# Kernel optimization log

Hardware: AMD Instinct MI355X
Metric: run time of the kernel (lower is better)

The kernel has to match this reference:

```python
import jax, jax.numpy as jnp
import numpy as np

B = 64        # graphs per batch
N0 = 131072   # total nodes (2048 per graph)
E = 1048576   # total edges (within-graph)
H = 128       # hidden_size
C = 7         # class_num (input feature dim)
EPS = 1e-5


def setup_inputs() -> dict:
    key = jax.random.key(0)
    ks = jax.random.split(key, 16)
    n0 = N0 // B
    x = jax.random.normal(ks[0], (N0, C), dtype=jnp.float32)
    # within-graph random edges: edge e belongs to graph e // (E//B)
    g = jnp.repeat(jnp.arange(B, dtype=jnp.int32), E // B)
    row = jax.random.randint(ks[1], (E,), 0, n0, dtype=jnp.int32) + g * n0
    col = jax.random.randint(ks[2], (E,), 0, n0, dtype=jnp.int32) + g * n0
    edge_index = jnp.stack([row, col], axis=0)
    batch = jnp.repeat(jnp.arange(B, dtype=jnp.int32), n0)
    s = 0.05
    params = dict(
        Wc1=jax.random.normal(ks[3], (C, H), jnp.float32) * s,     # conv1 weight
        Wc=jax.random.normal(ks[4], (3, H, H), jnp.float32) * s,   # conv2-4 weights
        bc=jax.random.normal(ks[5], (4, H), jnp.float32) * s,      # conv biases
        Wf=jax.random.normal(ks[6], (4, H, H), jnp.float32) * s,   # fc weights
        bf=jax.random.normal(ks[7], (4, H), jnp.float32) * s,      # fc biases
        bn_g=jnp.ones((4, H), jnp.float32),                        # BN gamma
        bn_b=jnp.zeros((4, H), jnp.float32),                       # BN beta
        Ws1=jax.random.normal(ks[8], (4, H, 1), jnp.float32) * s,  # SAG GraphConv root weight
        Ws2=jax.random.normal(ks[9], (4, H, 1), jnp.float32) * s,  # SAG GraphConv neighbor weight
        bs=jax.random.normal(ks[10], (4, 1), jnp.float32) * s,     # SAG GraphConv bias
    )
    return dict(x=x, edge_index=edge_index, batch=batch, **params)


def _gcn_conv(x, W, b, row, col, m, N):
    # PyG GCNConv with self loops: out_i = sum_{j->i} h_j / sqrt(d_i d_j) + h_i / d_i + b
    h = x @ W
    deg = jax.ops.segment_sum(m, col, num_segments=N) + 1.0  # +1 for self loop
    dis = jax.lax.rsqrt(deg)
    norm = dis[row] * dis[col] * m  # masked-out edges contribute 0
    agg = jax.ops.segment_sum(h[row] * norm[:, None], col, num_segments=N)
    return agg + h * (dis * dis)[:, None] + b


def _sag_score(x, W1, W2, b, row, col, m, N):
    # GraphConv(H, 1, aggr='add'): score_i = W1^T x_i + W2^T sum_{j->i} x_j + b
    nbr = jax.ops.segment_sum(x[row] * m[:, None], col, num_segments=N)
    return (x @ W1 + nbr @ W2 + b).reshape(-1)


def _bn(x, g, b):
    mu = jnp.mean(x, axis=0)
    var = jnp.mean((x - mu) ** 2, axis=0)  # biased, matches torch BN training
    return (x - mu) * jax.lax.rsqrt(var + EPS) * g + b


def reference(x, edge_index, batch, Wc1, Wc, bc, Wf, bf, bn_g, bn_b, Ws1, Ws2, bs):
    row, col = edge_index[0], edge_index[1]
    m = jnp.ones(row.shape, x.dtype)  # edge validity mask (static-size edge list)
    n = x.shape[0] // B               # nodes per graph (equal-size graphs)
    for i in range(4):
        N = B * n
        W = Wc1 if i == 0 else Wc[i - 1]
        h = _gcn_conv(x, W, bc[i], row, col, m, N)
        h = jax.nn.relu(h @ Wf[i] + bf[i])
        h = _bn(h, bn_g[i], bn_b[i])
        # SAGPooling(ratio=0.5): per-graph top-k by GraphConv score, x *= tanh(score)
        score = _sag_score(h, Ws1[i], Ws2[i], bs[i], row, col, m, N)
        k = n // 2
        _, idx = jax.lax.top_k(score.reshape(B, n), k)  # [B, k] per-graph indices
        perm = (idx + jnp.arange(B, dtype=idx.dtype)[:, None] * n).reshape(-1)
        x = h[perm] * jnp.tanh(score[perm])[:, None]
        # re-index edges; mask edges touching removed nodes
        inv = jnp.full((N,), -1, dtype=row.dtype).at[perm].set(
            jnp.arange(B * k, dtype=row.dtype))
        nr, nc = inv[row], inv[col]
        valid = (nr >= 0) & (nc >= 0)
        m = m * valid.astype(m.dtype)
        row = jnp.where(valid, nr, 0)
        col = jnp.where(valid, nc, 0)
        n = k
    # global_mean_pool over block-structured batch -> [B, H]
    return x.reshape(B, n, -1).mean(axis=1)
```

## Files before the change

kernel.cpp:

```cpp
#include <hip/hip_runtime.h>
#include <cstdint>

#define HB 128
#define NB 64
#define NE 1048576
#define EG (NE / 256)
#define XP 132

typedef float v2f __attribute__((ext_vector_type(2)));

__global__ __launch_bounds__(256) void init_edges_k(const int* __restrict__ ei,
    int* __restrict__ row, int* __restrict__ col, int* __restrict__ gcnt0,
    int* __restrict__ ecnt0, int E) {
  int e = blockIdx.x * blockDim.x + threadIdx.x;
  if (e < E) { row[e] = ei[e]; col[e] = ei[E + e]; }
  if (blockIdx.x == 0) {
    if (threadIdx.x < NB) gcnt0[threadIdx.x] = E / NB;
    if (threadIdx.x == 0) *ecnt0 = E;
  }
}

__global__ __launch_bounds__(256) void conv_fc0_k(const float* __restrict__ aggx,
    const float* __restrict__ Wc1, const float* __restrict__ bc0,
    const float* __restrict__ Wf, const float* __restrict__ bf0,
    float* __restrict__ out, int N, float* __restrict__ stat) {
  __shared__ float lt[64][128];
  __shared__ float laggx[64][8];
  __shared__ float lwc1[7 * 128];
  float2 (*red)[128] = (float2(*)[128])lt;
  int tid = threadIdx.x;
  int tx = tid & 31, ty = tid >> 5;
  long rowbase = (long)blockIdx.x * 64;
  for (int i = tid; i < 7 * 32; i += 256)
    ((float4*)lwc1)[i] = ((const float4*)Wc1)[i];
  if (tid < 128) {
    int lr = tid >> 1, lq = (tid & 1) * 4;
    *(float4*)&laggx[lr][lq] = *(const float4*)(aggx + (rowbase + lr) * 8 + lq);
  }
  __syncthreads();
  float4 tacc[8];
  float4 bcv = ((const float4*)bc0)[tx];
  #pragma unroll
  for (int r = 0; r < 8; ++r) tacc[r] = bcv;
  #pragma unroll
  for (int k = 0; k < 7; ++k) {
    float4 wv = ((float4*)lwc1)[k * 32 + tx];
    #pragma unroll
    for (int r = 0; r < 8; ++r) {
      float xv = laggx[ty + 8 * r][k];
      tacc[r].x += xv * wv.x; tacc[r].y += xv * wv.y;
      tacc[r].z += xv * wv.z; tacc[r].w += xv * wv.w;
    }
  }
  #pragma unroll
  for (int r = 0; r < 8; ++r)
    *(float4*)&lt[ty + 8 * r][4 * tx] = tacc[r];
  __syncthreads();
  v2f acc2[16];
  #pragma unroll
  for (int r = 0; r < 16; ++r) acc2[r] = (v2f){0.f, 0.f};
  for (int kc = 0; kc < 16; ++kc) {
    float4 wreg[8];
    #pragma unroll
    for (int k = 0; k < 8; ++k)
      wreg[k] = *(const float4*)(Wf + (size_t)(kc * 8 + k) * HB + 4 * tx);
    #pragma unroll
    for (int kk = 0; kk < 8; kk += 4) {
      float4 xreg[8];
      #pragma unroll
      for (int r = 0; r < 8; ++r)
        xreg[r] = *(const float4*)&lt[ty + 8 * r][kc * 8 + kk];
      #pragma unroll
      for (int k2 = 0; k2 < 4; ++k2) {
        float4 wv = wreg[kk + k2];
        v2f wlo = {wv.x, wv.y}, whi = {wv.z, wv.w};
        #pragma unroll
        for (int r = 0; r < 8; ++r) {
          float xv = ((const float*)&xreg[r])[k2];
          v2f xvv = {xv, xv};
          acc2[2 * r]     += xvv * wlo;
          acc2[2 * r + 1] += xvv * whi;
        }
      }
    }
  }
  float4 bv = ((const float4*)bf0)[tx];
  float4 psum = make_float4(0.f, 0.f, 0.f, 0.f);
  float4 psq  = make_float4(0.f, 0.f, 0.f, 0.f);
  __syncthreads();
  #pragma unroll
  for (int r = 0; r < 8; ++r) {
    float4 v;
    v.x = fmaxf(acc2[2 * r].x + bv.x, 0.f);
    v.y = fmaxf(acc2[2 * r].y + bv.y, 0.f);
    v.z = fmaxf(acc2[2 * r + 1].x + bv.z, 0.f);
    v.w = fmaxf(acc2[2 * r + 1].y + bv.w, 0.f);
    psum.x += v.x; psum.y += v.y; psum.z += v.z; psum.w += v.w;
    psq.x += v.x * v.x; psq.y += v.y * v.y;
    psq.z += v.z * v.z; psq.w += v.w * v.w;
    *(float4*)(out + (size_t)(rowbase + ty + 8 * r) * HB + 4 * tx) = v;
  }
  red[ty][4 * tx + 0] = make_float2(psum.x, psq.x);
  red[ty][4 * tx + 1] = make_float2(psum.y, psq.y);
  red[ty][4 * tx + 2] = make_float2(psum.z, psq.z);
  red[ty][4 * tx + 3] = make_float2(psum.w, psq.w);
  __syncthreads();
  if (tid < 128) {
    float s = 0.f, q = 0.f;
    #pragma unroll
    for (int t = 0; t < 8; ++t) { s += red[t][tid].x; q += red[t][tid].y; }
    float* st = stat + ((blockIdx.x & 7) << 8);
    atomicAdd(&st[tid], s);
    atomicAdd(&st[128 + tid], q);
  }
}

__global__ __launch_bounds__(256) void conv_fc_k(const float* __restrict__ Ap,
    const float* __restrict__ bnsc, const int* __restrict__ sel,
    const float* __restrict__ scale, const int* __restrict__ srow,
    const float* __restrict__ snorm, const int* __restrict__ off,
    const float* __restrict__ dis, const float* __restrict__ Wc,
    const float* __restrict__ bc0, const float* __restrict__ Wf,
    const float* __restrict__ bf0, float* __restrict__ out, int N,
    float* __restrict__ stat) {
  __shared__ float buf[64][XP];
  float2 (*red)[128] = (float2(*)[128])buf;
  int tid = threadIdx.x;
  int tx = tid & 31, ty = tid >> 5;
  long cpx = gridDim.x >> 3;
  long bb = ((long)blockIdx.x & 7) * cpx + ((long)blockIdx.x >> 3);
  long rowbase = bb * 64;
  {
    int r = tid >> 2;
    int chq = (tid & 3) * 32;
    int node = rowbase + r;
    float4 av[8], bv8[8];
    #pragma unroll
    for (int q = 0; q < 8; ++q) {
      av[q]  = *(const float4*)(bnsc + chq + 4 * q);
      bv8[q] = *(const float4*)(bnsc + 128 + chq + 4 * q);
    }
    int e0 = off[node], e1 = off[node + 1];
    float dv = dis[node];
    float4 acc[8];
    {
      float sc = scale[node] * dv * dv;
      const float* xr = Ap + (size_t)sel[node] * HB + chq;
      #pragma unroll
      for (int q = 0; q < 8; ++q) {
        float4 v = *(const float4*)(xr + 4 * q);
        acc[q].x = (v.x * av[q].x + bv8[q].x) * sc;
        acc[q].y = (v.y * av[q].y + bv8[q].y) * sc;
        acc[q].z = (v.z * av[q].z + bv8[q].z) * sc;
        acc[q].w = (v.w * av[q].w + bv8[q].w) * sc;
      }
    }
    for (int j = e0; j < e1; ++j) {
      int srcn = srow[j];
      float sc = snorm[j] * scale[srcn];
      const float* xr = Ap + (size_t)sel[srcn] * HB + chq;
      #pragma unroll
      for (int q = 0; q < 8; ++q) {
        float4 v = *(const float4*)(xr + 4 * q);
        acc[q].x += (v.x * av[q].x + bv8[q].x) * sc;
        acc[q].y += (v.y * av[q].y + bv8[q].y) * sc;
        acc[q].z += (v.z * av[q].z + bv8[q].z) * sc;
        acc[q].w += (v.w * av[q].w + bv8[q].w) * sc;
      }
    }
    #pragma unroll
    for (int q = 0; q < 8; ++q) *(float4*)&buf[r][chq + 4 * q] = acc[q];
  }
  __syncthreads();
  {
    float4 bcv = ((const float4*)bc0)[tx];
    v2f acc2[16];
    #pragma unroll
    for (int r = 0; r < 8; ++r) {
      acc2[2 * r]     = (v2f){bcv.x, bcv.y};
      acc2[2 * r + 1] = (v2f){bcv.z, bcv.w};
    }
    for (int kc = 0; kc < 16; ++kc) {
      float4 wreg[8];
      #pragma unroll
      for (int k = 0; k < 8; ++k)
        wreg[k] = *(const float4*)(Wc + (size_t)(kc * 8 + k) * HB + 4 * tx);
      #pragma unroll
      for (int kk = 0; kk < 8; kk += 4) {
        float4 xreg[8];
        #pragma unroll
        for (int r = 0; r < 8; ++r)
          xreg[r] = *(const float4*)&buf[ty + 8 * r][kc * 8 + kk];
        #pragma unroll
        for (int k2 = 0; k2 < 4; ++k2) {
          float4 wv = wreg[kk + k2];
          v2f wlo = {wv.x, wv.y}, whi = {wv.z, wv.w};
          #pragma unroll
          for (int r = 0; r < 8; ++r) {
            float xv = ((const float*)&xreg[r])[k2];
            v2f xvv = {xv, xv};
            acc2[2 * r]     += xvv * wlo;
            acc2[2 * r + 1] += xvv * whi;
          }
        }
      }
    }
    __syncthreads();
    #pragma unroll
    for (int r = 0; r < 8; ++r) {
      float4 v;
      v.x = acc2[2 * r].x;     v.y = acc2[2 * r].y;
      v.z = acc2[2 * r + 1].x; v.w = acc2[2 * r + 1].y;
      *(float4*)&buf[ty + 8 * r][4 * tx] = v;
    }
  }
  __syncthreads();
  v2f acc2[16];
  #pragma unroll
  for (int r = 0; r < 16; ++r) acc2[r] = (v2f){0.f, 0.f};
  for (int kc = 0; kc < 16; ++kc) {
    float4 wreg[8];
    #pragma unroll
    for (int k = 0; k < 8; ++k)
      wreg[k] = *(const float4*)(Wf + (size_t)(kc * 8 + k) * HB + 4 * tx);
    #pragma unroll
    for (int kk = 0; kk < 8; kk += 4) {
      float4 xreg[8];
      #pragma unroll
      for (int r = 0; r < 8; ++r)
        xreg[r] = *(const float4*)&buf[ty + 8 * r][kc * 8 + kk];
      #pragma unroll
      for (int k2 = 0; k2 < 4; ++k2) {
        float4 wv = wreg[kk + k2];
        v2f wlo = {wv.x, wv.y}, whi = {wv.z, wv.w};
        #pragma unroll
        for (int r = 0; r < 8; ++r) {
          float xv = ((const float*)&xreg[r])[k2];
          v2f xvv = {xv, xv};
          acc2[2 * r]     += xvv * wlo;
          acc2[2 * r + 1] += xvv * whi;
        }
      }
    }
  }
  float4 bv = ((const float4*)bf0)[tx];
  float4 psum = make_float4(0.f, 0.f, 0.f, 0.f);
  float4 psq  = make_float4(0.f, 0.f, 0.f, 0.f);
  __syncthreads();
  #pragma unroll
  for (int r = 0; r < 8; ++r) {
    float4 v;
    v.x = fmaxf(acc2[2 * r].x + bv.x, 0.f);
    v.y = fmaxf(acc2[2 * r].y + bv.y, 0.f);
    v.z = fmaxf(acc2[2 * r + 1].x + bv.z, 0.f);
    v.w = fmaxf(acc2[2 * r + 1].y + bv.w, 0.f);
    psum.x += v.x; psum.y += v.y; psum.z += v.z; psum.w += v.w;
    psq.x += v.x * v.x; psq.y += v.y * v.y;
    psq.z += v.z * v.z; psq.w += v.w * v.w;
    *(float4*)(out + (size_t)(rowbase + ty + 8 * r) * HB + 4 * tx) = v;
  }
  red[ty][4 * tx + 0] = make_float2(psum.x, psq.x);
  red[ty][4 * tx + 1] = make_float2(psum.y, psq.y);
  red[ty][4 * tx + 2] = make_float2(psum.z, psq.z);
  red[ty][4 * tx + 3] = make_float2(psum.w, psq.w);
  __syncthreads();
  if (tid < 128) {
    float s = 0.f, q = 0.f;
    #pragma unroll
    for (int t = 0; t < 8; ++t) { s += red[t][tid].x; q += red[t][tid].y; }
    float* st = stat + (((int)blockIdx.x & 7) << 8);
    atomicAdd(&st[tid], s);
    atomicAdd(&st[128 + tid], q);
  }
}

__global__ __launch_bounds__(1024) void csr_build_k(const int* __restrict__ row,
    const int* __restrict__ col, const int* __restrict__ gcnt,
    float* __restrict__ dis, int* __restrict__ off, int* __restrict__ srow,
    float* __restrict__ snorm, int n) {
  extern __shared__ int lds[];
  int* ldeg = lds;
  int* lsa  = lds + n;
  int* lsb  = lds + 2 * n;
  float* ldis = (float*)(lds + 3 * n);
  __shared__ int e01[2];
  int g = blockIdx.x, tid = threadIdx.x;
  if (tid == 0) {
    int s = 0;
    for (int gg = 0; gg < g; ++gg) s += gcnt[gg];
    e01[0] = s; e01[1] = s + gcnt[g];
  }
  int base = g * n;
  for (int i = tid; i < n; i += 1024) ldeg[i] = 0;
  __syncthreads();
  int e0 = e01[0], e1 = e01[1];
  for (int e = e0 + tid; e < e1; e += 1024) atomicAdd(&ldeg[col[e] - base], 1);
  __syncthreads();
  for (int i = tid; i < n; i += 1024) {
    int d = ldeg[i];
    ldis[i] = rsqrtf((float)d + 1.f);
    lsa[i] = d;
  }
  __syncthreads();
  int* src = lsa; int* dst = lsb;
  for (int o = 1; o < n; o <<= 1) {
    for (int i = tid; i < n; i += 1024) dst[i] = src[i] + ((i >= o) ? src[i - o] : 0);
    __syncthreads();
    int* t = src; src = dst; dst = t;
  }
  for (int i = tid; i < n; i += 1024) {
    int d = ldeg[i];
    int ex = src[i] - d;
    off[base + i] = e0 + ex;
    ldeg[i] = ex;
    dis[base + i] = ldis[i];
  }
  if (tid == 0) off[base + n] = e1;
  __syncthreads();
  for (int e = e0 + tid; e < e1; e += 1024) {
    int r = row[e], c = col[e];
    int lc = c - base;
    int p = e0 + atomicAdd(&ldeg[lc], 1);
    srow[p] = r;
    snorm[p] = ldis[r - base] * ldis[lc];
  }
}

__global__ __launch_bounds__(256) void agg7_k(const float* __restrict__ x,
    const int* __restrict__ srow, const float* __restrict__ snorm,
    const int* __restrict__ off, const float* __restrict__ dis,
    float* __restrict__ aggx, int N) {
  int cpx = gridDim.x >> 3;
  int b = blockIdx.x;
  int bid = (b & 7) * cpx + (b >> 3);
  int gid = bid * 256 + threadIdx.x;
  int node = gid >> 3, c = gid & 7;
  if (node >= N) return;
  float acc = 0.f;
  if (c < 7) {
    int s = off[node], e = off[node + 1];
    for (int j = s; j < e; ++j) acc += x[(size_t)srow[j] * 7 + c] * snorm[j];
    float d = dis[node];
    acc += x[(size_t)node * 7 + c] * d * d;
  }
  aggx[(size_t)node * 8 + c] = acc;
}

__global__ __launch_bounds__(128) void bnfin_k(const float* __restrict__ stat8,
    const float* __restrict__ g, const float* __restrict__ b,
    float* __restrict__ sc, int N) {
  int c = threadIdx.x;
  if (c < 128) {
    float s = 0.f, q = 0.f;
    #pragma unroll
    for (int sh = 0; sh < 8; ++sh) {
      s += stat8[sh * 256 + c];
      q += stat8[sh * 256 + 128 + c];
    }
    float mu = s / N;
    float var = q / N - mu * mu;
    float a = g[c] * rsqrtf(var + 1e-5f);
    sc[c] = a;
    sc[128 + c] = b[c] - mu * a;
  }
}

__global__ __launch_bounds__(256) void score_prep_k(const float* __restrict__ h,
    const float* __restrict__ sc, const float* __restrict__ w1,
    const float* __restrict__ w2, float* __restrict__ selfs,
    float* __restrict__ t2, int N) {
  int gid = blockIdx.x * blockDim.x + threadIdx.x;
  int node = gid >> 6;
  if (node >= N) return;
  int lane = gid & 63, c = lane * 2;
  float2 v = *(const float2*)(h + (size_t)node * HB + c);
  v.x = v.x * sc[c] + sc[128 + c];
  v.y = v.y * sc[c + 1] + sc[128 + c + 1];
  float s1 = v.x * w1[c] + v.y * w1[c + 1];
  float s2 = v.x * w2[c] + v.y * w2[c + 1];
  #pragma unroll
  for (int off = 32; off > 0; off >>= 1) {
    s1 += __shfl_xor(s1, off);
    s2 += __shfl_xor(s2, off);
  }
  if (lane == 0) { selfs[node] = s1; t2[node] = s2; }
}

__global__ __launch_bounds__(256) void score_k(const float* __restrict__ selfs,
    const float* __restrict__ t2, const int* __restrict__ srow,
    const int* __restrict__ off, const float* __restrict__ bs,
    float* __restrict__ score, int N) {
  int i = blockIdx.x * blockDim.x + threadIdx.x;
  if (i >= N) return;
  float s = selfs[i] + bs[0];
  int e0 = off[i], e1 = off[i + 1];
  for (int j = e0; j < e1; ++j) s += t2[srow[j]];
  score[i] = s;
}

__global__ __launch_bounds__(256) void rank_topk_k(const float* __restrict__ score,
    int* __restrict__ inv, int* __restrict__ sel, float* __restrict__ scale,
    int n, int k, int bpg) {
  extern __shared__ float ls[];
  int g = blockIdx.x / bpg, sub = blockIdx.x % bpg;
  int tid = threadIdx.x;
  const float* sg = score + (size_t)g * n;
  for (int i = tid; i < n; i += 256) ls[i] = sg[i];
  __syncthreads();
  int i0 = sub * 256 + tid;
  float s0 = ls[i0];
  int r0 = 0;
  for (int jb = 0; jb < n; jb += 4) {
    float4 v = *(const float4*)(ls + jb);
    r0 += (v.x > s0) || (v.x == s0 && (jb + 0) < i0);
    r0 += (v.y > s0) || (v.y == s0 && (jb + 1) < i0);
    r0 += (v.z > s0) || (v.z == s0 && (jb + 2) < i0);
    r0 += (v.w > s0) || (v.w == s0 && (jb + 3) < i0);
  }
  if (r0 < k) {
    inv[(size_t)g * n + i0] = g * k + r0;
    sel[(size_t)g * k + r0] = g * n + i0;
    scale[(size_t)g * k + r0] = tanhf(s0);
  } else inv[(size_t)g * n + i0] = -1;
}

__global__ __launch_bounds__(256) void gather_x_k(const float* __restrict__ h,
    const float* __restrict__ bnsc, const int* __restrict__ sel,
    const float* __restrict__ scale, float* __restrict__ xout, int M) {
  int gid = blockIdx.x * blockDim.x + threadIdx.x;
  int r = gid >> 5;
  if (r >= M) return;
  int ch = (gid & 31) * 4;
  int old = sel[r];
  float sc = scale[r];
  float4 v = *(const float4*)(h + (size_t)old * HB + ch);
  float4 a = *(const float4*)(bnsc + ch);
  float4 b = *(const float4*)(bnsc + 128 + ch);
  v.x = (v.x * a.x + b.x) * sc; v.y = (v.y * a.y + b.y) * sc;
  v.z = (v.z * a.z + b.z) * sc; v.w = (v.w * a.w + b.w) * sc;
  *(float4*)(xout + (size_t)r * HB + ch) = v;
}

__global__ __launch_bounds__(256) void cmpA_k(const int* __restrict__ row,
    const int* __restrict__ col, const int* __restrict__ inv,
    const int* __restrict__ ecnt, int* __restrict__ bcnt) {
  int e = blockIdx.x * 256 + threadIdx.x;
  bool valid = false;
  if (e < *ecnt) {
    int nr = inv[row[e]], nc = inv[col[e]];
    valid = (nr >= 0) && (nc >= 0);
  }
  unsigned long long mask = __ballot(valid);
  __shared__ int ws[4];
  int lane = threadIdx.x & 63, wid = threadIdx.x >> 6;
  if (lane == 0) ws[wid] = __popcll(mask);
  __syncthreads();
  if (threadIdx.x == 0) bcnt[blockIdx.x] = ws[0] + ws[1] + ws[2] + ws[3];
}

__global__ __launch_bounds__(1024) void cmpB_k(const int* __restrict__ bcnt,
    int* __restrict__ bbase, int* __restrict__ total) {
  __shared__ int s[1024];
  int tid = threadIdx.x;
  int v0 = bcnt[4 * tid], v1 = bcnt[4 * tid + 1];
  int v2 = bcnt[4 * tid + 2], v3 = bcnt[4 * tid + 3];
  int tsum = v0 + v1 + v2 + v3;
  s[tid] = tsum; __syncthreads();
  for (int o = 1; o < 1024; o <<= 1) {
    int t = (tid >= o) ? s[tid - o] : 0;
    __syncthreads();
    s[tid] += t;
    __syncthreads();
  }
  int base = s[tid] - tsum;
  bbase[4 * tid] = base;
  bbase[4 * tid + 1] = base + v0;
  bbase[4 * tid + 2] = base + v0 + v1;
  bbase[4 * tid + 3] = base + v0 + v1 + v2;
  if (tid == 1023) *total = s[1023];
}

__global__ __launch_bounds__(256) void cmpC_k(const int* __restrict__ row,
    const int* __restrict__ col, const int* __restrict__ inv,
    const int* __restrict__ ecnt, const int* __restrict__ bbase,
    int* __restrict__ nrow, int* __restrict__ ncol, int* __restrict__ gcnt,
    int khalf) {
  int e = blockIdx.x * 256 + threadIdx.x;
  bool valid = false; int nr = 0, nc = 0;
  if (e < *ecnt) {
    nr = inv[row[e]]; nc = inv[col[e]];
    valid = (nr >= 0) && (nc >= 0);
  }
  unsigned long long mask = __ballot(valid);
  int lane = threadIdx.x & 63, wid = threadIdx.x >> 6;
  __shared__ int ws[4];
  __shared__ int lg[NB];
  if (threadIdx.x < NB) lg[threadIdx.x] = 0;
  if (lane == 0) ws[wid] = __popcll(mask);
  __syncthreads();
  if (threadIdx.x == 0) {
    int a = ws[0], b = ws[1], c2 = ws[2];
    ws[0] = 0; ws[1] = a; ws[2] = a + b; ws[3] = a + b + c2;
  }
  __syncthreads();
  if (valid) {
    unsigned long long lt = ((unsigned long long)1 << lane) - 1;
    int pos = bbase[blockIdx.x] + ws[wid] + (int)__popcll(mask & lt);
    nrow[pos] = nr;
    ncol[pos] = nc;
    atomicAdd(&lg[nc / khalf], 1);
  }
  __syncthreads();
  if (threadIdx.x < NB && lg[threadIdx.x]) atomicAdd(&gcnt[threadIdx.x], lg[threadIdx.x]);
}

__global__ __launch_bounds__(128) void pool_k(const float* __restrict__ x,
    float* __restrict__ out, int n) {
  int g = blockIdx.x, c = threadIdx.x;
  float s = 0.f;
  for (int r = 0; r < n; ++r) s += x[((size_t)g * n + r) * HB + c];
  out[g * HB + c] = s / n;
}

extern "C" void kernel_launch(void* const* d_in, const int* in_sizes, int n_in,
                              void* d_out, int out_size, void* d_ws, size_t ws_size,
                              hipStream_t stream) {
  const float* x_in = (const float*)d_in[0];
  const int*   ei   = (const int*)d_in[1];
  const float* Wc1  = (const float*)d_in[3];
  const float* Wc   = (const float*)d_in[4];
  const float* bc   = (const float*)d_in[5];
  const float* Wf   = (const float*)d_in[6];
  const float* bf   = (const float*)d_in[7];
  const float* bng  = (const float*)d_in[8];
  const float* bnb  = (const float*)d_in[9];
  const float* Ws1  = (const float*)d_in[10];
  const float* Ws2  = (const float*)d_in[11];
  const float* bs   = (const float*)d_in[12];

  const int N0 = 131072, E = NE;
  char* p = (char*)d_ws;
  auto alloc = [&](size_t bytes) -> char* {
    char* r = p; p += (bytes + 255) & ~(size_t)255; return r;
  };
  float* A    = (float*)alloc((size_t)N0 * HB * 4);
  float* Bb   = (float*)alloc((size_t)N0 * HB * 4);
  float* Cc   = (float*)alloc((size_t)(N0 / 2) * HB * 4);
  float* aggx = (float*)alloc((size_t)N0 * 8 * 4);
  int*   rowA = (int*)alloc((size_t)E * 4);
  int*   colA = (int*)alloc((size_t)E * 4);
  int*   rowB = (int*)alloc((size_t)E * 4);
  int*   colB = (int*)alloc((size_t)E * 4);
  float* dis  = (float*)alloc((size_t)N0 * 4);
  float* selfs= (float*)alloc((size_t)N0 * 4);
  float* t2v  = (float*)alloc((size_t)N0 * 4);
  float* score= (float*)alloc((size_t)N0 * 4);
  int*   inv  = (int*)alloc((size_t)N0 * 4);
  int*   off  = (int*)alloc((size_t)(N0 + 1) * 4);
  int*   sel  = (int*)alloc((size_t)(N0 / 2) * 4);
  float* scale= (float*)alloc((size_t)(N0 / 2) * 4);
  int*   bcnt = (int*)alloc((size_t)EG * 4);
  int*   bbase= (int*)alloc((size_t)EG * 4);
  int*   gcntL= (int*)alloc(4 * NB * 4);
  float* stat8= (float*)alloc(4 * 8 * 256 * 4);
  float* bnsc = (float*)alloc(256 * 4);
  int*   ecnt = (int*)alloc(2 * 4);

  hipMemsetAsync(stat8, 0, 4 * 8 * 256 * 4, stream);
  hipMemsetAsync(gcntL, 0, 4 * NB * 4, stream);

  init_edges_k<<<E / 256, 256, 0, stream>>>(ei, rowA, colA, gcntL, ecnt, E);

  int* rowCur = rowA; int* colCur = colA;
  int* rowNxt = rowB; int* colNxt = colB;
  int* ecntCur = ecnt; int* ecntNxt = ecnt + 1;

  int n = 2048;
  for (int i = 0; i < 4; ++i) {
    int N = NB * n, khalf = n >> 1;
    float* statL = stat8 + (size_t)i * 8 * 256;
    const float* Xin  = (i == 2) ? Bb : A;
    float*       Xout = (i == 0 || i == 2) ? A : Bb;
    int*   srow  = rowNxt;
    float* snorm = (float*)colNxt;
    csr_build_k<<<NB, 1024, (size_t)16 * n, stream>>>(
        rowCur, colCur, gcntL + i * NB, dis, off, srow, snorm, n);
    if (i == 0) {
      agg7_k<<<N / 32, 256, 0, stream>>>(x_in, srow, snorm, off, dis, aggx, N);
      conv_fc0_k<<<N / 64, 256, 0, stream>>>(aggx, Wc1, bc, Wf, bf, Xout, N, statL);
    } else {
      conv_fc_k<<<N / 64, 256, 0, stream>>>(
          Xin, bnsc, sel, scale, srow, snorm, off, dis,
          Wc + (size_t)(i - 1) * HB * HB, bc + (size_t)i * HB,
          Wf + (size_t)i * HB * HB, bf + (size_t)i * HB, Xout, N, statL);
    }
    bnfin_k<<<1, 128, 0, stream>>>(statL, bng + (size_t)i * HB, bnb + (size_t)i * HB, bnsc, N);
    score_prep_k<<<N / 4, 256, 0, stream>>>(
        Xout, bnsc, Ws1 + (size_t)i * HB, Ws2 + (size_t)i * HB, selfs, t2v, N);
    score_k<<<(N + 255) / 256, 256, 0, stream>>>(selfs, t2v, srow, off, bs + i, score, N);
    int bpg = n / 256;
    rank_topk_k<<<NB * bpg, 256, (size_t)n * 4, stream>>>(
        score, inv, sel, scale, n, khalf, bpg);
    if (i < 3) {
      cmpA_k<<<EG, 256, 0, stream>>>(rowCur, colCur, inv, ecntCur, bcnt);
      cmpB_k<<<1, 1024, 0, stream>>>(bcnt, bbase, ecntNxt);
      cmpC_k<<<EG, 256, 0, stream>>>(rowCur, colCur, inv, ecntCur, bbase,
                                     rowNxt, colNxt, gcntL + (i + 1) * NB, khalf);
      int* t;
      t = rowCur; rowCur = rowNxt; rowNxt = t;
      t = colCur; colCur = colNxt; colNxt = t;
      t = ecntCur; ecntCur = ecntNxt; ecntNxt = t;
    } else {
      gather_x_k<<<(NB * khalf) / 8, 256, 0, stream>>>(
          Xout, bnsc, sel, scale, Cc, NB * khalf);
    }
    n = khalf;
  }
  pool_k<<<NB, 128, 0, stream>>>(Cc, (float*)d_out, n);
}
```

Baseline: 601.6 us.

## Store compacted edges in fixed per-graph slabs with atomic allocation

Replaces the global three-kernel edge compaction (count, single-block scan, scatter) with one kernel. It compacts edges into a fixed 16384-entry slab per graph and reserves output positions with a per-block atomicAdd on the graph's counter. The CSR build now reads edge ranges straight from slab offsets, and node end offsets are stored in a separate offe array, so the serial prefix over graph counts goes away. In exchange, edge order within a slab is no longer deterministic across blocks, which can change floating-point summation order. Blocks whose slab range lies past the live edge count return early.

```diff
diff --git a/kernel.cpp b/kernel.cpp
--- a/kernel.cpp
+++ b/kernel.cpp
@@ -4,20 +4,16 @@
 #define HB 128
 #define NB 64
 #define NE 1048576
-#define EG (NE / 256)
+#define SLAB 16384
 #define XP 132
 
 typedef float v2f __attribute__((ext_vector_type(2)));
 
 __global__ __launch_bounds__(256) void init_edges_k(const int* __restrict__ ei,
-    int* __restrict__ row, int* __restrict__ col, int* __restrict__ gcnt0,
-    int* __restrict__ ecnt0, int E) {
+    int* __restrict__ row, int* __restrict__ col, int* __restrict__ gcnt0, int E) {
   int e = blockIdx.x * blockDim.x + threadIdx.x;
   if (e < E) { row[e] = ei[e]; col[e] = ei[E + e]; }
-  if (blockIdx.x == 0) {
-    if (threadIdx.x < NB) gcnt0[threadIdx.x] = E / NB;
-    if (threadIdx.x == 0) *ecnt0 = E;
-  }
+  if (blockIdx.x == 0 && threadIdx.x < NB) gcnt0[threadIdx.x] = SLAB;
 }
 
 __global__ __launch_bounds__(256) void conv_fc0_k(const float* __restrict__ aggx,
@@ -119,10 +115,10 @@
     const float* __restrict__ bnsc, const int* __restrict__ sel,
     const float* __restrict__ scale, const int* __restrict__ srow,
     const float* __restrict__ snorm, const int* __restrict__ off,
-    const float* __restrict__ dis, const float* __restrict__ Wc,
-    const float* __restrict__ bc0, const float* __restrict__ Wf,
-    const float* __restrict__ bf0, float* __restrict__ out, int N,
-    float* __restrict__ stat) {
+    const int* __restrict__ offe, const float* __restrict__ dis,
+    const float* __restrict__ Wc, const float* __restrict__ bc0,
+    const float* __restrict__ Wf, const float* __restrict__ bf0,
+    float* __restrict__ out, int N, float* __restrict__ stat) {
   __shared__ float buf[64][XP];
   float2 (*red)[128] = (float2(*)[128])buf;
   int tid = threadIdx.x;
@@ -140,7 +136,7 @@
       av[q]  = *(const float4*)(bnsc + chq + 4 * q);
       bv8[q] = *(const float4*)(bnsc + 128 + chq + 4 * q);
     }
-    int e0 = off[node], e1 = off[node + 1];
+    int e0 = off[node], e1 = offe[node];
     float dv = dis[node];
     float4 acc[8];
     {
@@ -276,24 +272,18 @@
 
 __global__ __launch_bounds__(1024) void csr_build_k(const int* __restrict__ row,
     const int* __restrict__ col, const int* __restrict__ gcnt,
-    float* __restrict__ dis, int* __restrict__ off, int* __restrict__ srow,
-    float* __restrict__ snorm, int n) {
+    float* __restrict__ dis, int* __restrict__ off, int* __restrict__ offe,
+    int* __restrict__ srow, float* __restrict__ snorm, int n) {
   extern __shared__ int lds[];
   int* ldeg = lds;
   int* lsa  = lds + n;
   int* lsb  = lds + 2 * n;
   float* ldis = (float*)(lds + 3 * n);
-  __shared__ int e01[2];
   int g = blockIdx.x, tid = threadIdx.x;
-  if (tid == 0) {
-    int s = 0;
-    for (int gg = 0; gg < g; ++gg) s += gcnt[gg];
-    e01[0] = s; e01[1] = s + gcnt[g];
-  }
+  int e0 = g * SLAB, e1 = e0 + gcnt[g];
   int base = g * n;
   for (int i = tid; i < n; i += 1024) ldeg[i] = 0;
   __syncthreads();
-  int e0 = e01[0], e1 = e01[1];
   for (int e = e0 + tid; e < e1; e += 1024) atomicAdd(&ldeg[col[e] - base], 1);
   __syncthreads();
   for (int i = tid; i < n; i += 1024) {
@@ -311,11 +301,11 @@
   for (int i = tid; i < n; i += 1024) {
     int d = ldeg[i];
     int ex = src[i] - d;
-    off[base + i] = e0 + ex;
+    off[base + i]  = e0 + ex;
+    offe[base + i] = e0 + ex + d;
     ldeg[i] = ex;
     dis[base + i] = ldis[i];
   }
-  if (tid == 0) off[base + n] = e1;
   __syncthreads();
   for (int e = e0 + tid; e < e1; e += 1024) {
     int r = row[e], c = col[e];
@@ -328,8 +318,8 @@
 
 __global__ __launch_bounds__(256) void agg7_k(const float* __restrict__ x,
     const int* __restrict__ srow, const float* __restrict__ snorm,
-    const int* __restrict__ off, const float* __restrict__ dis,
-    float* __restrict__ aggx, int N) {
+    const int* __restrict__ off, const int* __restrict__ offe,
+    const float* __restrict__ dis, float* __restrict__ aggx, int N) {
   int cpx = gridDim.x >> 3;
   int b = blockIdx.x;
   int bid = (b & 7) * cpx + (b >> 3);
@@ -338,7 +328,7 @@
   if (node >= N) return;
   float acc = 0.f;
   if (c < 7) {
-    int s = off[node], e = off[node + 1];
+    int s = off[node], e = offe[node];
     for (int j = s; j < e; ++j) acc += x[(size_t)srow[j] * 7 + c] * snorm[j];
     float d = dis[node];
     acc += x[(size_t)node * 7 + c] * d * d;
@@ -388,12 +378,12 @@
 
 __global__ __launch_bounds__(256) void score_k(const float* __restrict__ selfs,
     const float* __restrict__ t2, const int* __restrict__ srow,
-    const int* __restrict__ off, const float* __restrict__ bs,
-    float* __restrict__ score, int N) {
+    const int* __restrict__ off, const int* __restrict__ offe,
+    const float* __restrict__ bs, float* __restrict__ score, int N) {
   int i = blockIdx.x * blockDim.x + threadIdx.x;
   if (i >= N) return;
   float s = selfs[i] + bs[0];
-  int e0 = off[i], e1 = off[i + 1];
+  int e0 = off[i], e1 = offe[i];
   for (int j = e0; j < e1; ++j) s += t2[srow[j]];
   score[i] = s;
 }
@@ -441,77 +431,39 @@
   *(float4*)(xout + (size_t)r * HB + ch) = v;
 }
 
-__global__ __launch_bounds__(256) void cmpA_k(const int* __restrict__ row,
+__global__ __launch_bounds__(256) void cmp_k(const int* __restrict__ row,
     const int* __restrict__ col, const int* __restrict__ inv,
-    const int* __restrict__ ecnt, int* __restrict__ bcnt) {
-  int e = blockIdx.x * 256 + threadIdx.x;
-  bool valid = false;
-  if (e < *ecnt) {
-    int nr = inv[row[e]], nc = inv[col[e]];
-    valid = (nr >= 0) && (nc >= 0);
-  }
-  unsigned long long mask = __ballot(valid);
-  __shared__ int ws[4];
-  int lane = threadIdx.x & 63, wid = threadIdx.x >> 6;
-  if (lane == 0) ws[wid] = __popcll(mask);
-  __syncthreads();
-  if (threadIdx.x == 0) bcnt[blockIdx.x] = ws[0] + ws[1] + ws[2] + ws[3];
-}
-
-__global__ __launch_bounds__(1024) void cmpB_k(const int* __restrict__ bcnt,
-    int* __restrict__ bbase, int* __restrict__ total) {
-  __shared__ int s[1024];
-  int tid = threadIdx.x;
-  int v0 = bcnt[4 * tid], v1 = bcnt[4 * tid + 1];
-  int v2 = bcnt[4 * tid + 2], v3 = bcnt[4 * tid + 3];
-  int tsum = v0 + v1 + v2 + v3;
-  s[tid] = tsum; __syncthreads();
-  for (int o = 1; o < 1024; o <<= 1) {
-    int t = (tid >= o) ? s[tid - o] : 0;
-    __syncthreads();
-    s[tid] += t;
-    __syncthreads();
-  }
-  int base = s[tid] - tsum;
-  bbase[4 * tid] = base;
-  bbase[4 * tid + 1] = base + v0;
-  bbase[4 * tid + 2] = base + v0 + v1;
-  bbase[4 * tid + 3] = base + v0 + v1 + v2;
-  if (tid == 1023) *total = s[1023];
-}
-
-__global__ __launch_bounds__(256) void cmpC_k(const int* __restrict__ row,
-    const int* __restrict__ col, const int* __restrict__ inv,
-    const int* __restrict__ ecnt, const int* __restrict__ bbase,
-    int* __restrict__ nrow, int* __restrict__ ncol, int* __restrict__ gcnt,
-    int khalf) {
-  int e = blockIdx.x * 256 + threadIdx.x;
+    const int* __restrict__ gcntCur, int* __restrict__ nrow,
+    int* __restrict__ ncol, int* __restrict__ gcntNxt) {
+  int g = blockIdx.x >> 6;
+  int eloc = ((blockIdx.x & 63) << 8) + threadIdx.x;
+  int cnt = gcntCur[g];
+  if (((blockIdx.x & 63) << 8) >= cnt) return;
+  long e = (long)g * SLAB + eloc;
   bool valid = false; int nr = 0, nc = 0;
-  if (e < *ecnt) {
+  if (eloc < cnt) {
     nr = inv[row[e]]; nc = inv[col[e]];
     valid = (nr >= 0) && (nc >= 0);
   }
   unsigned long long mask = __ballot(valid);
   int lane = threadIdx.x & 63, wid = threadIdx.x >> 6;
   __shared__ int ws[4];
-  __shared__ int lg[NB];
-  if (threadIdx.x < NB) lg[threadIdx.x] = 0;
+  __shared__ int base;
   if (lane == 0) ws[wid] = __popcll(mask);
   __syncthreads();
   if (threadIdx.x == 0) {
-    int a = ws[0], b = ws[1], c2 = ws[2];
+    int a = ws[0], b = ws[1], c2 = ws[2], d = ws[3];
+    int tot = a + b + c2 + d;
+    base = tot ? atomicAdd(&gcntNxt[g], tot) : 0;
     ws[0] = 0; ws[1] = a; ws[2] = a + b; ws[3] = a + b + c2;
   }
   __syncthreads();
   if (valid) {
     unsigned long long lt = ((unsigned long long)1 << lane) - 1;
-    int pos = bbase[blockIdx.x] + ws[wid] + (int)__popcll(mask & lt);
-    nrow[pos] = nr;
-    ncol[pos] = nc;
-    atomicAdd(&lg[nc / khalf], 1);
-  }
-  __syncthreads();
-  if (threadIdx.x < NB && lg[threadIdx.x]) atomicAdd(&gcnt[threadIdx.x], lg[threadIdx.x]);
+    long o = (long)g * SLAB + base + ws[wid] + (int)__popcll(mask & lt);
+    nrow[o] = nr;
+    ncol[o] = nc;
+  }
 }
 
 __global__ __launch_bounds__(128) void pool_k(const float* __restrict__ x,
@@ -556,24 +508,21 @@
   float* t2v  = (float*)alloc((size_t)N0 * 4);
   float* score= (float*)alloc((size_t)N0 * 4);
   int*   inv  = (int*)alloc((size_t)N0 * 4);
-  int*   off  = (int*)alloc((size_t)(N0 + 1) * 4);
+  int*   off  = (int*)alloc((size_t)N0 * 4);
+  int*   offe = (int*)alloc((size_t)N0 * 4);
   int*   sel  = (int*)alloc((size_t)(N0 / 2) * 4);
   float* scale= (float*)alloc((size_t)(N0 / 2) * 4);
-  int*   bcnt = (int*)alloc((size_t)EG * 4);
-  int*   bbase= (int*)alloc((size_t)EG * 4);
   int*   gcntL= (int*)alloc(4 * NB * 4);
   float* stat8= (float*)alloc(4 * 8 * 256 * 4);
   float* bnsc = (float*)alloc(256 * 4);
-  int*   ecnt = (int*)alloc(2 * 4);
 
   hipMemsetAsync(stat8, 0, 4 * 8 * 256 * 4, stream);
   hipMemsetAsync(gcntL, 0, 4 * NB * 4, stream);
 
-  init_edges_k<<<E / 256, 256, 0, stream>>>(ei, rowA, colA, gcntL, ecnt, E);
+  init_edges_k<<<E / 256, 256, 0, stream>>>(ei, rowA, colA, gcntL, E);
 
   int* rowCur = rowA; int* colCur = colA;
   int* rowNxt = rowB; int* colNxt = colB;
-  int* ecntCur = ecnt; int* ecntNxt = ecnt + 1;
 
   int n = 2048;
   for (int i = 0; i < 4; ++i) {
@@ -584,32 +533,30 @@
     int*   srow  = rowNxt;
     float* snorm = (float*)colNxt;
     csr_build_k<<<NB, 1024, (size_t)16 * n, stream>>>(
-        rowCur, colCur, gcntL + i * NB, dis, off, srow, snorm, n);
+        rowCur, colCur, gcntL + i * NB, dis, off, offe, srow, snorm, n);
     if (i == 0) {
-      agg7_k<<<N / 32, 256, 0, stream>>>(x_in, srow, snorm, off, dis, aggx, N);
+      agg7_k<<<N / 32, 256, 0, stream>>>(x_in, srow, snorm, off, offe, dis, aggx, N);
       conv_fc0_k<<<N / 64, 256, 0, stream>>>(aggx, Wc1, bc, Wf, bf, Xout, N, statL);
     } else {
       conv_fc_k<<<N / 64, 256, 0, stream>>>(
-          Xin, bnsc, sel, scale, srow, snorm, off, dis,
+          Xin, bnsc, sel, scale, srow, snorm, off, offe, dis,
           Wc + (size_t)(i - 1) * HB * HB, bc + (size_t)i * HB,
           Wf + (size_t)i * HB * HB, bf + (size_t)i * HB, Xout, N, statL);
     }
     bnfin_k<<<1, 128, 0, stream>>>(statL, bng + (size_t)i * HB, bnb + (size_t)i * HB, bnsc, N);
     score_prep_k<<<N / 4, 256, 0, stream>>>(
         Xout, bnsc, Ws1 + (size_t)i * HB, Ws2 + (size_t)i * HB, selfs, t2v, N);
-    score_k<<<(N + 255) / 256, 256, 0, stream>>>(selfs, t2v, srow, off, bs + i, score, N);
+    score_k<<<(N + 255) / 256, 256, 0, stream>>>(
+        selfs, t2v, srow, off, offe, bs + i, score, N);
     int bpg = n / 256;
     rank_topk_k<<<NB * bpg, 256, (size_t)n * 4, stream>>>(
         score, inv, sel, scale, n, khalf, bpg);
     if (i < 3) {
-      cmpA_k<<<EG, 256, 0, stream>>>(rowCur, colCur, inv, ecntCur, bcnt);
-      cmpB_k<<<1, 1024, 0, stream>>>(bcnt, bbase, ecntNxt);
-      cmpC_k<<<EG, 256, 0, stream>>>(rowCur, colCur, inv, ecntCur, bbase,
-                                     rowNxt, colNxt, gcntL + (i + 1) * NB, khalf);
+      cmp_k<<<NB * 64, 256, 0, stream>>>(rowCur, colCur, inv, gcntL + i * NB,
+                                         rowNxt, colNxt, gcntL + (i + 1) * NB);
       int* t;
       t = rowCur; rowCur = rowNxt; rowNxt = t;
       t = colCur; colCur = colNxt; colNxt = t;
-      t = ecntCur; ecntCur = ecntNxt; ecntNxt = t;
     } else {
       gather_x_k<<<(NB * khalf) / 8, 256, 0, stream>>>(
           Xout, bnsc, sel, scale, Cc, NB * khalf);
```

New measurement: 582.4 us (median of 2 runs). 3.2% less time.
